# Kernel tuning notes

Hardware: AMD Instinct MI355X
Metric: run time of the kernel (lower is better)

Reference implementation:

```python
import jax, jax.numpy as jnp
import numpy as np

B, C, L = 16, 256, 4096
P, Q = 100, 20


def setup_inputs() -> dict:
    key = jax.random.key(0)
    k1, k2, k3, k4 = jax.random.split(key, 4)
    X = jax.random.normal(k1, (B, C, L), dtype=jnp.float32)
    projections = jax.random.normal(k2, (P, C), dtype=jnp.float32)
    # min < max per projection. Projected values ~ N(0, sqrt(C)), so scale ~ sqrt(C).
    scale = jnp.sqrt(jnp.float32(C))
    min_vals = -scale * (1.0 + jax.random.uniform(k3, (P,), dtype=jnp.float32))
    max_vals = scale * (1.0 + jax.random.uniform(k4, (P,), dtype=jnp.float32))
    return {"X": X, "projections": projections, "min_vals": min_vals, "max_vals": max_vals}


def reference(X, projections, min_vals, max_vals):
    # conv1d with kernel size 1 == per-position projection: [B,C,L] x [P,C] -> [B,P,L]
    a = jnp.einsum('bcl,pc->bpl', X, projections)
    # all quantile thresholds at once: thr[p,q] = min + (max-min)*(q+1)/(Q+1)
    fracs = (jnp.arange(1, Q + 1, dtype=jnp.float32)) / jnp.float32(Q + 1)  # [Q]
    thr = min_vals[:, None] + (max_vals - min_vals)[:, None] * fracs[None, :]  # [P,Q]
    # set[b,p,l,q] = a[b,p,l] < thr[p,q]
    set_ = (a[:, :, :, None] < thr[None, :, None, :]).astype(jnp.float32)  # [B,P,L,Q]
    cdf = jnp.mean(set_, axis=2)  # [B,P,Q]
    # transpose(2,1) -> [B,L,P,Q]; reshape -> [B,L,P*Q]; transpose(2,1) -> [B,P*Q,L]
    set_out = jnp.transpose(set_, (0, 2, 1, 3)).reshape(B, L, P * Q)
    set_out = jnp.transpose(set_out, (0, 2, 1))  # [B, P*Q, L]
    cdf_out = cdf.reshape(B, P * Q)
    return (cdf_out, set_out)
```

## Files before the change

kernel.cpp:

```cpp
#include <hip/hip_runtime.h>

#define Bsz 16
#define Cc  256
#define Ll  4096
#define Pp  100
#define Qq  20
#define LT  64
#define NLB (Ll / LT)
#define PPW 25
#define PQ  (Pp * Qq)

__global__ __launch_bounds__(256) void csf_main(
    const float* __restrict__ X,
    const float* __restrict__ proj,
    const float* __restrict__ mn,
    const float* __restrict__ mx,
    float* __restrict__ cdf,
    float* __restrict__ set_out,
    float* __restrict__ counts,
    int use_atomic) {
    const int lblk = blockIdx.x;
    const int b    = blockIdx.y;
    const int tid  = threadIdx.x;
    const int lane = tid & 63;
    const int pg   = __builtin_amdgcn_readfirstlane(tid >> 6);
    const int l    = lblk * LT + lane;

    const float* Xb = X + (size_t)b * Cc * Ll + l;
    const int p0 = pg * PPW;
    const float* pj = proj + (size_t)p0 * Cc;

    float acc[PPW];
#pragma unroll
    for (int i = 0; i < PPW; i++) acc[i] = 0.0f;

    for (int c = 0; c < Cc; c += 8) {
        float x[8];
#pragma unroll
        for (int u = 0; u < 8; u++) x[u] = Xb[(size_t)(c + u) * Ll];
#pragma unroll
        for (int i = 0; i < PPW; i++) {
            const float* pr = pj + i * Cc + c;
            float a = acc[i];
#pragma unroll
            for (int u = 0; u < 8; u++) a = __builtin_fmaf(x[u], pr[u], a);
            acc[i] = a;
        }
    }

    float fr[Qq];
#pragma unroll
    for (int q = 0; q < Qq; q++) fr[q] = __fdiv_rn((float)(q + 1), 21.0f);

    float* ob = set_out + (size_t)b * PQ * Ll + l;
#pragma unroll 1
    for (int i = 0; i < PPW; i++) {
        const int p = p0 + i;
        const float a = acc[i];
        const float mnp = mn[p];
        const float mxp = mx[p];
        const float d = __fsub_rn(mxp, mnp);
#pragma unroll
        for (int q = 0; q < Qq; q++) {
            const float thr = __fadd_rn(mnp, __fmul_rn(d, fr[q]));
            const bool bit = a < thr;
            const unsigned long long m = __ballot(bit);
            ob[(size_t)(p * Qq + q) * Ll] = bit ? 1.0f : 0.0f;
            if (lane == 0) {
                const float cnt = (float)__popcll(m);
                if (use_atomic) {
                    atomicAdd(&cdf[(size_t)b * PQ + p * Qq + q],
                              cnt * (1.0f / (float)Ll));
                } else {
                    counts[((size_t)(b * NLB + lblk)) * PQ + p * Qq + q] = cnt;
                }
            }
        }
    }
}

__global__ void csf_reduce(const float* __restrict__ counts,
                           float* __restrict__ cdf) {
    int idx = blockIdx.x * blockDim.x + threadIdx.x;
    if (idx >= Bsz * PQ) return;
    int b = idx / PQ;
    int r = idx % PQ;
    float s = 0.0f;
    for (int k = 0; k < NLB; k++)
        s += counts[((size_t)(b * NLB + k)) * PQ + r];
    cdf[idx] = s * (1.0f / (float)Ll);
}

extern "C" void kernel_launch(void* const* d_in, const int* in_sizes, int n_in,
                              void* d_out, int out_size, void* d_ws, size_t ws_size,
                              hipStream_t stream) {
    const float* X    = (const float*)d_in[0];
    const float* proj = (const float*)d_in[1];
    const float* mn   = (const float*)d_in[2];
    const float* mx   = (const float*)d_in[3];

    float* cdf     = (float*)d_out;
    float* set_out = cdf + (size_t)Bsz * PQ;

    const size_t counts_bytes = (size_t)Bsz * NLB * PQ * sizeof(float);

    int use_atomic;
    float* counts = nullptr;
    if (ws_size >= counts_bytes) {
        use_atomic = 0;
        counts = (float*)d_ws;
    } else {
        use_atomic = 1;
    }

    if (use_atomic) hipMemsetAsync(cdf, 0, (size_t)Bsz * PQ * sizeof(float), stream);

    dim3 grid(NLB, Bsz);
    csf_main<<<grid, 256, 0, stream>>>(X, proj, mn, mx, cdf, set_out, counts, use_atomic);

    if (!use_atomic)
        csf_reduce<<<(Bsz * PQ + 255) / 256, 256, 0, stream>>>(counts, cdf);
}
```

Measured before the change: 677.6 us.

## Retile over L and projection groups with vectorized nontemporal stores and atomic cdf

```diff
diff --git a/kernel.cpp b/kernel.cpp
--- a/kernel.cpp
+++ b/kernel.cpp
@@ -5,10 +5,14 @@
 #define Ll  4096
 #define Pp  100
 #define Qq  20
-#define LT  64
-#define NLB (Ll / LT)
-#define PPW 25
 #define PQ  (Pp * Qq)
+
+#define LTILE 1024
+#define NLT   (Ll / LTILE)
+#define GP    10
+#define NPG   (Pp / GP)
+
+typedef float f32x4 __attribute__((ext_vector_type(4)));
 
 __global__ __launch_bounds__(256) void csf_main(
     const float* __restrict__ X,
@@ -16,35 +20,32 @@
     const float* __restrict__ mn,
     const float* __restrict__ mx,
     float* __restrict__ cdf,
-    float* __restrict__ set_out,
-    float* __restrict__ counts,
-    int use_atomic) {
-    const int lblk = blockIdx.x;
-    const int b    = blockIdx.y;
-    const int tid  = threadIdx.x;
-    const int lane = tid & 63;
-    const int pg   = __builtin_amdgcn_readfirstlane(tid >> 6);
-    const int l    = lblk * LT + lane;
+    float* __restrict__ set_out) {
+    const int lt  = blockIdx.x;
+    const int pg  = blockIdx.y;
+    const int b   = blockIdx.z;
+    const int tid = threadIdx.x;
+    const int l0  = lt * LTILE + tid * 4;
+    const int p0  = __builtin_amdgcn_readfirstlane(pg * GP);
 
-    const float* Xb = X + (size_t)b * Cc * Ll + l;
-    const int p0 = pg * PPW;
-    const float* pj = proj + (size_t)p0 * Cc;
+    const float* Xb = X + (size_t)b * Cc * Ll + l0;
 
-    float acc[PPW];
+    float acc[GP][4];
 #pragma unroll
-    for (int i = 0; i < PPW; i++) acc[i] = 0.0f;
+    for (int i = 0; i < GP; i++)
+#pragma unroll
+        for (int k = 0; k < 4; k++) acc[i][k] = 0.0f;
 
-    for (int c = 0; c < Cc; c += 8) {
-        float x[8];
+#pragma unroll 4
+    for (int c = 0; c < Cc; c++) {
+        const f32x4 x = *(const f32x4*)(Xb + (size_t)c * Ll);
 #pragma unroll
-        for (int u = 0; u < 8; u++) x[u] = Xb[(size_t)(c + u) * Ll];
-#pragma unroll
-        for (int i = 0; i < PPW; i++) {
-            const float* pr = pj + i * Cc + c;
-            float a = acc[i];
-#pragma unroll
-            for (int u = 0; u < 8; u++) a = __builtin_fmaf(x[u], pr[u], a);
-            acc[i] = a;
+        for (int i = 0; i < GP; i++) {
+            const float w = proj[(size_t)(p0 + i) * Cc + c];
+            acc[i][0] = __builtin_fmaf(x.x, w, acc[i][0]);
+            acc[i][1] = __builtin_fmaf(x.y, w, acc[i][1]);
+            acc[i][2] = __builtin_fmaf(x.z, w, acc[i][2]);
+            acc[i][3] = __builtin_fmaf(x.w, w, acc[i][3]);
         }
     }
 
@@ -52,43 +53,36 @@
 #pragma unroll
     for (int q = 0; q < Qq; q++) fr[q] = __fdiv_rn((float)(q + 1), 21.0f);
 
-    float* ob = set_out + (size_t)b * PQ * Ll + l;
+    float* ob = set_out + (size_t)b * PQ * Ll + l0;
+    const bool lane0 = ((tid & 63) == 0);
+
 #pragma unroll 1
-    for (int i = 0; i < PPW; i++) {
+    for (int i = 0; i < GP; i++) {
         const int p = p0 + i;
-        const float a = acc[i];
         const float mnp = mn[p];
         const float mxp = mx[p];
         const float d = __fsub_rn(mxp, mnp);
 #pragma unroll
         for (int q = 0; q < Qq; q++) {
             const float thr = __fadd_rn(mnp, __fmul_rn(d, fr[q]));
-            const bool bit = a < thr;
-            const unsigned long long m = __ballot(bit);
-            ob[(size_t)(p * Qq + q) * Ll] = bit ? 1.0f : 0.0f;
-            if (lane == 0) {
-                const float cnt = (float)__popcll(m);
-                if (use_atomic) {
-                    atomicAdd(&cdf[(size_t)b * PQ + p * Qq + q],
-                              cnt * (1.0f / (float)Ll));
-                } else {
-                    counts[((size_t)(b * NLB + lblk)) * PQ + p * Qq + q] = cnt;
-                }
+            const bool b0 = acc[i][0] < thr;
+            const bool b1 = acc[i][1] < thr;
+            const bool b2 = acc[i][2] < thr;
+            const bool b3 = acc[i][3] < thr;
+            f32x4 o;
+            o.x = b0 ? 1.0f : 0.0f;
+            o.y = b1 ? 1.0f : 0.0f;
+            o.z = b2 ? 1.0f : 0.0f;
+            o.w = b3 ? 1.0f : 0.0f;
+            __builtin_nontemporal_store(o, (f32x4*)(ob + (size_t)(p * Qq + q) * Ll));
+            const int cnt = __popcll(__ballot(b0)) + __popcll(__ballot(b1))
+                          + __popcll(__ballot(b2)) + __popcll(__ballot(b3));
+            if (lane0) {
+                atomicAdd(&cdf[(size_t)b * PQ + p * Qq + q],
+                          (float)cnt * (1.0f / (float)Ll));
             }
         }
     }
-}
-
-__global__ void csf_reduce(const float* __restrict__ counts,
-                           float* __restrict__ cdf) {
-    int idx = blockIdx.x * blockDim.x + threadIdx.x;
-    if (idx >= Bsz * PQ) return;
-    int b = idx / PQ;
-    int r = idx % PQ;
-    float s = 0.0f;
-    for (int k = 0; k < NLB; k++)
-        s += counts[((size_t)(b * NLB + k)) * PQ + r];
-    cdf[idx] = s * (1.0f / (float)Ll);
 }
 
 extern "C" void kernel_launch(void* const* d_in, const int* in_sizes, int n_in,
@@ -102,22 +96,8 @@
     float* cdf     = (float*)d_out;
     float* set_out = cdf + (size_t)Bsz * PQ;
 
-    const size_t counts_bytes = (size_t)Bsz * NLB * PQ * sizeof(float);
+    (void)hipMemsetAsync(cdf, 0, (size_t)Bsz * PQ * sizeof(float), stream);
 
-    int use_atomic;
-    float* counts = nullptr;
-    if (ws_size >= counts_bytes) {
-        use_atomic = 0;
-        counts = (float*)d_ws;
-    } else {
-        use_atomic = 1;
-    }
-
-    if (use_atomic) hipMemsetAsync(cdf, 0, (size_t)Bsz * PQ * sizeof(float), stream);
-
-    dim3 grid(NLB, Bsz);
-    csf_main<<<grid, 256, 0, stream>>>(X, proj, mn, mx, cdf, set_out, counts, use_atomic);
-
-    if (!use_atomic)
-        csf_reduce<<<(Bsz * PQ + 255) / 256, 256, 0, stream>>>(counts, cdf);
+    dim3 grid(NLT, NPG, Bsz);
+    csf_main<<<grid, 256, 0, stream>>>(X, proj, mn, mx, cdf, set_out);
 }
```

New measurement: 603.1 us. -11.0%, faster.
